# Optimization experiments

Hardware: AMD Instinct MI355X
Metric: run time of the kernel (lower is better)

## Reference

```python
import jax, jax.numpy as jnp
import numpy as np

B, V, J = 64, 8, 17
H = 256  # square heatmap; original clamps both coords to heatmap.shape[3]-1


def setup_inputs() -> dict:
    key = jax.random.key(0)
    k1, k2 = jax.random.split(key)
    # keypoint coords roughly spanning the heatmap grid (some out-of-range to hit clamp)
    keypoints_gt = jax.random.uniform(k1, (B, V, J, 2), dtype=jnp.float32, minval=-2.0, maxval=float(H) + 2.0)
    # heatmap values strictly positive so -log is finite (original assumes probabilities)
    heatmap = jax.random.uniform(k2, (B, V, 1, H, H), dtype=jnp.float32, minval=1e-3, maxval=1.0)
    return {"keypoints_gt": keypoints_gt, "heatmap": heatmap}


def reference(keypoints_gt, heatmap):
    b_, v_, j_, _ = keypoints_gt.shape
    hdim = heatmap.shape[3]
    # ceil then clamp to [0, H-1] (matches min(max(int(ceil(v)),0),H-1))
    idx = jnp.ceil(keypoints_gt).astype(jnp.int32)
    x = jnp.clip(idx[..., 0], 0, hdim - 1)  # [B,V,J]
    y = jnp.clip(idx[..., 1], 0, hdim - 1)  # [B,V,J]
    hm = heatmap[:, :, 0]  # [B,V,H,W]
    bi = jnp.arange(b_)[:, None, None]
    vi = jnp.arange(v_)[None, :, None]
    vals = hm[bi, vi, y, x]  # [B,V,J] gathered heatmap probabilities
    return jnp.mean(-jnp.log(vals))
```

## Files before the change

### kernel.cpp

```cpp
#include <hip/hip_runtime.h>

#define BB 64
#define VV 8
#define JJ 17
#define HH 256
#define NN (BB * VV * JJ)

__global__ __launch_bounds__(1024) void HeatmapCELoss_kernel(
    const float* __restrict__ kp,
    const float* __restrict__ hm,
    float* __restrict__ out)
{
    const int tid = threadIdx.x;
    float sum = 0.0f;

    for (int i = tid; i < NN; i += 1024) {
        float2 k = ((const float2*)kp)[i];
        int x = (int)ceilf(k.x);
        int y = (int)ceilf(k.y);
        x = min(max(x, 0), HH - 1);
        y = min(max(y, 0), HH - 1);
        int bv = i / JJ;
        float val = hm[((size_t)bv * HH + (size_t)y) * HH + (size_t)x];
        sum += -__logf(val);
    }

    #pragma unroll
    for (int off = 32; off > 0; off >>= 1)
        sum += __shfl_down(sum, off, 64);

    __shared__ float ws[16];
    const int wave = tid >> 6;
    if ((tid & 63) == 0) ws[wave] = sum;
    __syncthreads();

    if (wave == 0) {
        float s = (tid < 16) ? ws[tid] : 0.0f;
        #pragma unroll
        for (int off = 8; off > 0; off >>= 1)
            s += __shfl_down(s, off, 64);
        if (tid == 0) out[0] = s * (1.0f / (float)NN);
    }
}

extern "C" void kernel_launch(void* const* d_in, const int* in_sizes, int n_in,
                              void* d_out, int out_size, void* d_ws, size_t ws_size,
                              hipStream_t stream) {
    const float* kp = (const float*)d_in[0];
    const float* hm = (const float*)d_in[1];
    float* out = (float*)d_out;

    HeatmapCELoss_kernel<<<1, 1024, 0, stream>>>(kp, hm, out);
}
```

Baseline: 180.7 us.

## Split gather across many blocks with a separate reduction kernel

Replaces the single 1024-thread block with 136 one-wave blocks. Each block gathers one heatmap value per thread, takes the log, and writes its partial sum to workspace. A second single-wave kernel then sums the 136 partials. This spreads the latency-bound random gathers across many compute units instead of one, at the cost of an extra kernel launch and a round trip through global memory.

```diff
diff --git a/kernel.cpp b/kernel.cpp
--- a/kernel.cpp
+++ b/kernel.cpp
@@ -5,42 +5,45 @@
 #define JJ 17
 #define HH 256
 #define NN (BB * VV * JJ)
+#define NBLK (NN / 64)
 
-__global__ __launch_bounds__(1024) void HeatmapCELoss_kernel(
+__global__ __launch_bounds__(64) void HeatmapCELoss_gather(
     const float* __restrict__ kp,
     const float* __restrict__ hm,
-    float* __restrict__ out)
+    float* __restrict__ ws)
 {
-    const int tid = threadIdx.x;
-    float sum = 0.0f;
+    const int i = blockIdx.x * 64 + threadIdx.x;
 
-    for (int i = tid; i < NN; i += 1024) {
-        float2 k = ((const float2*)kp)[i];
-        int x = (int)ceilf(k.x);
-        int y = (int)ceilf(k.y);
-        x = min(max(x, 0), HH - 1);
-        y = min(max(y, 0), HH - 1);
-        int bv = i / JJ;
-        float val = hm[((size_t)bv * HH + (size_t)y) * HH + (size_t)x];
-        sum += -__logf(val);
-    }
+    float2 k = ((const float2*)kp)[i];
+    int x = (int)ceilf(k.x);
+    int y = (int)ceilf(k.y);
+    x = min(max(x, 0), HH - 1);
+    y = min(max(y, 0), HH - 1);
+    int bv = i / JJ;
+
+    float val = hm[((size_t)bv * HH + (size_t)y) * HH + (size_t)x];
+    float s = -__logf(val);
 
     #pragma unroll
     for (int off = 32; off > 0; off >>= 1)
-        sum += __shfl_down(sum, off, 64);
+        s += __shfl_down(s, off, 64);
 
-    __shared__ float ws[16];
-    const int wave = tid >> 6;
-    if ((tid & 63) == 0) ws[wave] = sum;
-    __syncthreads();
+    if (threadIdx.x == 0) ws[blockIdx.x] = s;
+}
 
-    if (wave == 0) {
-        float s = (tid < 16) ? ws[tid] : 0.0f;
-        #pragma unroll
-        for (int off = 8; off > 0; off >>= 1)
-            s += __shfl_down(s, off, 64);
-        if (tid == 0) out[0] = s * (1.0f / (float)NN);
-    }
+__global__ __launch_bounds__(64) void HeatmapCELoss_reduce(
+    const float* __restrict__ ws,
+    float* __restrict__ out)
+{
+    const int t = threadIdx.x;
+    float s = ws[t] + ws[t + 64];
+    if (t < NBLK - 128) s += ws[t + 128];
+
+    #pragma unroll
+    for (int off = 32; off > 0; off >>= 1)
+        s += __shfl_down(s, off, 64);
+
+    if (t == 0) out[0] = s * (1.0f / (float)NN);
 }
 
 extern "C" void kernel_launch(void* const* d_in, const int* in_sizes, int n_in,
@@ -48,7 +51,9 @@
                               hipStream_t stream) {
     const float* kp = (const float*)d_in[0];
     const float* hm = (const float*)d_in[1];
+    float* ws  = (float*)d_ws;
     float* out = (float*)d_out;
 
-    HeatmapCELoss_kernel<<<1, 1024, 0, stream>>>(kp, hm, out);
+    HeatmapCELoss_gather<<<NBLK, 64, 0, stream>>>(kp, hm, ws);
+    HeatmapCELoss_reduce<<<1, 64, 0, stream>>>(ws, out);
 }
```

Result: faster. 162.2 us (-10.3%).
